# Kernel tuning notes

Hardware: AMD Instinct MI355X
Metric: run time of the kernel (lower is better)

Reference implementation:

```python
import jax, jax.numpy as jnp
import numpy as np
from jax import lax

BN_EPS = 1e-5

def conv_bn_prelu(x, w, b, scale, bias, a):
    # Conv2d(k=3, pad=1, stride=1) in NCHW / OIHW layout
    y = lax.conv_general_dilated(x, w, window_strides=(1, 1), padding='SAME',
                                 dimension_numbers=('NCHW', 'OIHW', 'NCHW'))
    y = y + b[None, :, None, None]
    # BatchNorm2d, training-mode batch statistics over (B, H, W)
    mean = jnp.mean(y, axis=(0, 2, 3), keepdims=True)
    var = jnp.var(y, axis=(0, 2, 3), keepdims=True)
    y = (y - mean) * lax.rsqrt(var + BN_EPS)
    y = y * scale[None, :, None, None] + bias[None, :, None, None]
    # PReLU with single shared slope parameter
    return jnp.where(y >= 0, y, a * y)

def setup_inputs() -> dict:
    key = jax.random.key(0)
    ks = jax.random.split(key, 7)
    B, C, H, W = 4, 64, 64, 64
    x = jax.random.normal(ks[0], (B, C, H, W), dtype=jnp.float32)
    conv_w = jax.random.normal(ks[1], (C, C, 3, 3), dtype=jnp.float32) * 0.05
    conv_b = jax.random.normal(ks[2], (C,), dtype=jnp.float32) * 0.05
    bn_scale = jax.random.uniform(ks[3], (C,), dtype=jnp.float32, minval=0.5, maxval=1.5)
    bn_bias = jax.random.normal(ks[4], (C,), dtype=jnp.float32) * 0.05
    prelu_a = jnp.full((1,), 0.25, dtype=jnp.float32)
    gamma = jax.random.normal(ks[5], (1,), dtype=jnp.float32)
    return {'x': x, 'conv_w': conv_w, 'conv_b': conv_b, 'bn_scale': bn_scale,
            'bn_bias': bn_bias, 'prelu_a': prelu_a, 'gamma': gamma}

def reference(x, conv_w, conv_b, bn_scale, bn_bias, prelu_a, gamma):
    B, C, H, W = x.shape
    N = H * W
    feat = conv_bn_prelu(x, conv_w, conv_b, bn_scale, bn_bias, prelu_a)  # (B,C,H,W)
    f = feat.reshape(B, C, N)  # proj_query = f^T, proj_key = f, proj_value = f
    # energy[b,i,j] = sum_c f[b,c,i] * f[b,c,j]  -> (B, N, N)
    energy = jnp.einsum('bci,bcj->bij', f, f)
    # energy_new = rowmax - energy, softmax over last dim
    energy_new = jnp.max(energy, axis=-1, keepdims=True) - energy
    attn = jax.nn.softmax(energy_new, axis=-1)
    # out = bmm(proj_value, attention^T): out[b,c,i] = sum_j f[b,c,j] * attn[b,i,j]
    out = jnp.einsum('bcj,bij->bci', f, attn).reshape(B, C, H, W)
    return gamma * out + feat
```

## Files before the change

### kernel.cpp

```cpp
#include <hip/hip_runtime.h>

constexpr int kB = 4, kC = 64, kH = 64, kW = 64, kN = kH * kW;
constexpr float kEps = 1e-5f;
constexpr float kQS = 1.2011224087864498f;

#if __has_builtin(__builtin_amdgcn_exp2f)
#define EXP2F(x) __builtin_amdgcn_exp2f(x)
#else
#define EXP2F(x) exp2f(x)
#endif

typedef __attribute__((ext_vector_type(8))) short short8;
typedef __attribute__((ext_vector_type(4))) float f32x4;
typedef unsigned short u16;

__device__ inline unsigned pkbf(float a, float b) {
  unsigned ua = __float_as_uint(a), ub = __float_as_uint(b);
  ua += 0x7fff + ((ua >> 16) & 1);
  ub += 0x7fff + ((ub >> 16) & 1);
  return (ua >> 16) | (ub & 0xffff0000u);
}

__global__ __launch_bounds__(256) void prep_w_kernel(const float* __restrict__ w,
                                                     u16* __restrict__ wA,
                                                     float* __restrict__ stat) {
  if (blockIdx.x == 0) {
    stat[threadIdx.x] = 0.f;
    stat[256 + threadIdx.x] = 0.f;
  }
  int idx = blockIdx.x * 256 + threadIdx.x;
  if (idx < 64 * 576) {
    int oc = idx / 576, r = idx - oc * 576;
    int khw = r >> 6, ic = r & 63;
    float v = w[(oc * 64 + ic) * 9 + khw];
    unsigned u = __float_as_uint(v);
    u += 0x7fff + ((u >> 16) & 1);
    wA[idx] = (u16)(u >> 16);
  }
}

__global__ __launch_bounds__(256) void conv_kernel(const float* __restrict__ x,
                                                   const u16* __restrict__ wA,
                                                   const float* __restrict__ bias,
                                                   float* __restrict__ y,
                                                   float* __restrict__ stat) {
  const int tid = threadIdx.x;
  const int lane = tid & 63;
  const int wv = tid >> 6;
  const int bx = blockIdx.x;
  const int b = bx >> 7;
  const int h = (bx & 127) >> 1;
  const int w0 = (bx & 1) * 32;
  const int lw = lane & 15, lg = lane >> 4;

  __shared__ __align__(16) u16 xt[3 * 40 * 64];

#pragma unroll
  for (int rep = 0; rep < 4; ++rep) {
    int idx = rep * 256 + tid;
    if (idx < 960) {
      int kh = idx / 320;
      int t = idx - kh * 320;
      int gw = t >> 5, icp = t & 31;
      int wb = w0 - 4 + gw * 4;
      int hh = h + kh - 1;
      float4 va = {0.f, 0.f, 0.f, 0.f}, vb = {0.f, 0.f, 0.f, 0.f};
      if (hh >= 0 && hh < 64 && wb >= 0 && wb < 64) {
        va = *(const float4*)&x[((b * 64 + icp * 2) * 64 + hh) * 64 + wb];
        vb = *(const float4*)&x[((b * 64 + icp * 2 + 1) * 64 + hh) * 64 + wb];
      }
      float av[4] = {va.x, va.y, va.z, va.w};
      float bv[4] = {vb.x, vb.y, vb.z, vb.w};
#pragma unroll
      for (int j = 0; j < 4; ++j) {
        int wc = gw * 4 + j;
        *(unsigned*)&xt[(kh * 40 + wc) * 64 + (((icp >> 2) ^ (wc & 7)) * 8 + (icp & 3) * 2)] =
            pkbf(av[j], bv[j]);
      }
    }
  }
  __syncthreads();

  const int oc0 = wv * 16;
  short8 af[18];
#pragma unroll
  for (int kc = 0; kc < 18; ++kc)
    af[kc] = *(const short8*)&wA[(oc0 + lw) * 576 + kc * 32 + lg * 8];

  f32x4 acc[2];
  acc[0] = (f32x4){0.f, 0.f, 0.f, 0.f};
  acc[1] = (f32x4){0.f, 0.f, 0.f, 0.f};
#pragma unroll
  for (int kc = 0; kc < 18; ++kc) {
    const int khw = kc >> 1;
    const int kh = khw / 3, kwv = khw % 3;
#pragma unroll
    for (int nt = 0; nt < 2; ++nt) {
      int wc = nt * 16 + lw + kwv + 3;
      short8 bf = *(const short8*)&xt[(kh * 40 + wc) * 64 + ((((kc & 1) * 4 + lg) ^ (wc & 7)) * 8)];
      acc[nt] = __builtin_amdgcn_mfma_f32_16x16x32_bf16(af[kc], bf, acc[nt], 0, 0, 0);
    }
  }

  float* st = stat + (bx & 3) * 128;
#pragma unroll
  for (int r = 0; r < 4; ++r) {
    const int oc = oc0 + lg * 4 + r;
    const float bz = bias[oc];
    float v0 = acc[0][r] + bz;
    float v1 = acc[1][r] + bz;
    y[((b * 64 + oc) * 64 + h) * 64 + w0 + lw] = v0;
    y[((b * 64 + oc) * 64 + h) * 64 + w0 + 16 + lw] = v1;
    float s = v0 + v1, q = v0 * v0 + v1 * v1;
#pragma unroll
    for (int m = 1; m < 16; m <<= 1) {
      s += __shfl_xor(s, m);
      q += __shfl_xor(q, m);
    }
    if (lw == 0) {
      atomicAdd(&st[oc], s);
      atomicAdd(&st[64 + oc], q);
    }
  }
}

__global__ __launch_bounds__(256) void pack_kernel(const float* __restrict__ y,
                                                   const float* __restrict__ stat,
                                                   const float* __restrict__ scale,
                                                   const float* __restrict__ bias,
                                                   const float* __restrict__ pa,
                                                   float* __restrict__ ABg,
                                                   u16* __restrict__ fbfA,
                                                   u16* __restrict__ fbfB) {
  __shared__ float ls[64 * 65];
  __shared__ float sAB[128];
  const int tid = threadIdx.x;
  const int b = blockIdx.x >> 6;
  const int n0 = (blockIdx.x & 63) << 6;
  if (tid < 64) {
    const float inv_n = 1.f / (float)(kB * kN);
    float ssum = stat[tid] + stat[128 + tid] + stat[256 + tid] + stat[384 + tid];
    float qsum = stat[64 + tid] + stat[192 + tid] + stat[320 + tid] + stat[448 + tid];
    float mean = ssum * inv_n;
    float var = qsum * inv_n - mean * mean;
    float A = scale[tid] * rsqrtf(var + kEps);
    float Bc = bias[tid] - mean * A;
    sAB[tid] = A;
    sAB[64 + tid] = Bc;
    ABg[tid] = A;
    ABg[64 + tid] = Bc;
  }
  __syncthreads();
  {
    const int c = tid >> 2, nj = (tid & 3) << 4;
    const float A = sAB[c], Bc = sAB[64 + c], a = pa[0];
    const float* yp = y + ((b * kC + c) * kN) + n0 + nj;
    float f[16];
#pragma unroll
    for (int v = 0; v < 4; ++v) {
      float4 xv = *(const float4*)(yp + v * 4);
      float t;
      t = fmaf(A, xv.x, Bc); f[v * 4 + 0] = t >= 0.f ? t : a * t;
      t = fmaf(A, xv.y, Bc); f[v * 4 + 1] = t >= 0.f ? t : a * t;
      t = fmaf(A, xv.z, Bc); f[v * 4 + 2] = t >= 0.f ? t : a * t;
      t = fmaf(A, xv.w, Bc); f[v * 4 + 3] = t >= 0.f ? t : a * t;
    }
#pragma unroll
    for (int v = 0; v < 16; ++v) ls[c * 65 + nj + v] = f[v];
  }
  __syncthreads();
  {
    int chunk = tid >> 5, pt = chunk >> 1, kc = chunk & 1;
    int lp2 = (tid & 31) * 2;
    u16* dst = fbfA + ((size_t)((b * 256 + (n0 >> 4) + pt) * 2 + kc)) * 512;
#pragma unroll
    for (int e = 0; e < 2; ++e) {
      int L = lp2 + e;
      int n = pt * 16 + (L & 15);
      int cb = kc * 32 + (L >> 4) * 8;
      float v[8];
#pragma unroll
      for (int r = 0; r < 8; ++r) v[r] = kQS * ls[(cb + r) * 65 + n];
      uint4 o = {pkbf(v[0], v[1]), pkbf(v[2], v[3]), pkbf(v[4], v[5]), pkbf(v[6], v[7])};
      *(uint4*)&dst[L * 8] = o;
    }
  }
  {
    int chunk = tid >> 5, jt = chunk >> 2, ct = chunk & 3;
    int lp2 = (tid & 31) * 2;
    u16* dst = fbfB + ((size_t)((b * 128 + (n0 >> 5) + jt) * 4 + ct)) * 512;
#pragma unroll
    for (int e = 0; e < 2; ++e) {
      int L = lp2 + e;
      int c = ct * 16 + (L & 15);
      int nb = jt * 32 + (L >> 4) * 8;
      float v[8];
#pragma unroll
      for (int r = 0; r < 8; ++r) v[r] = ls[c * 65 + nb + r];
      uint4 o = {pkbf(v[0], v[1]), pkbf(v[2], v[3]), pkbf(v[4], v[5]), pkbf(v[6], v[7])};
      *(uint4*)&dst[L * 8] = o;
    }
  }
}

__global__ __launch_bounds__(512, 1) void attn_kernel(const u16* __restrict__ fbfA,
                                                      const u16* __restrict__ fbfB,
                                                      const float* y,
                                                      const float* __restrict__ ABg,
                                                      const float* __restrict__ pa,
                                                      const float* __restrict__ gamma_p,
                                                      float* out) {
  const int tid = threadIdx.x;
  const int lane = tid & 63;
  const int w = tid >> 6;
  const int bx = blockIdx.x;
  const int b = bx >> 6, it4 = bx & 63;
  const int c15 = lane & 15, g = lane >> 4;

  __shared__ __align__(16) float Red[20480];
  u16* ps = (u16*)Red + w * 2560;
  const int pw_off = c15 * 40 + g * 4;
  const int pr_off = c15 * 40 + g * 8;

  const uint4* fA = (const uint4*)fbfA;
  const uint4* fB = (const uint4*)fbfB;

  uint4 qf[4][2];
#pragma unroll
  for (int it = 0; it < 4; ++it)
#pragma unroll
    for (int kc = 0; kc < 2; ++kc) {
      uint4 q = fA[(size_t)((b * 256 + it4 * 4 + it) * 2 + kc) * 64 + lane];
      q.x ^= 0x80008000u; q.y ^= 0x80008000u; q.z ^= 0x80008000u; q.w ^= 0x80008000u;
      qf[it][kc] = q;
    }

  const short8 ones = {0x3F80, 0x3F80, 0x3F80, 0x3F80, 0x3F80, 0x3F80, 0x3F80, 0x3F80};

  f32x4 oacc[4][4];
  f32x4 lacc[4];
#pragma unroll
  for (int it = 0; it < 4; ++it) {
    lacc[it] = (f32x4){0.f, 0.f, 0.f, 0.f};
#pragma unroll
    for (int ct = 0; ct < 4; ++ct) oacc[it][ct] = (f32x4){0.f, 0.f, 0.f, 0.f};
  }

#pragma unroll 2
  for (int jj2 = 0; jj2 < 16; ++jj2) {
    const int jj = jj2 * 8 + w;
    const int ca = (b * 256 + jj * 2) * 2;
    uint4 a00 = fA[(size_t)(ca + 0) * 64 + lane];
    uint4 a01 = fA[(size_t)(ca + 1) * 64 + lane];
    uint4 a10 = fA[(size_t)(ca + 2) * 64 + lane];
    uint4 a11 = fA[(size_t)(ca + 3) * 64 + lane];
    const int cb = (b * 128 + jj) * 4;
    uint4 v0 = fB[(size_t)(cb + 0) * 64 + lane];
    uint4 v1 = fB[(size_t)(cb + 1) * 64 + lane];
    uint4 v2 = fB[(size_t)(cb + 2) * 64 + lane];
    uint4 v3 = fB[(size_t)(cb + 3) * 64 + lane];

    f32x4 sv[2][4];
    __builtin_amdgcn_s_setprio(1);
#pragma unroll
    for (int it = 0; it < 4; ++it) {
      f32x4 z0 = (f32x4){0.f, 0.f, 0.f, 0.f};
      z0 = __builtin_amdgcn_mfma_f32_16x16x32_bf16(*(short8*)&a00, *(short8*)&qf[it][0], z0, 0, 0, 0);
      z0 = __builtin_amdgcn_mfma_f32_16x16x32_bf16(*(short8*)&a01, *(short8*)&qf[it][1], z0, 0, 0, 0);
      sv[0][it] = z0;
      f32x4 z1 = (f32x4){0.f, 0.f, 0.f, 0.f};
      z1 = __builtin_amdgcn_mfma_f32_16x16x32_bf16(*(short8*)&a10, *(short8*)&qf[it][0], z1, 0, 0, 0);
      z1 = __builtin_amdgcn_mfma_f32_16x16x32_bf16(*(short8*)&a11, *(short8*)&qf[it][1], z1, 0, 0, 0);
      sv[1][it] = z1;
    }
    __builtin_amdgcn_s_setprio(0);
#pragma unroll
    for (int it = 0; it < 4; ++it)
#pragma unroll
      for (int jt = 0; jt < 2; ++jt) {
        float p0 = EXP2F(sv[jt][it][0]);
        float p1 = EXP2F(sv[jt][it][1]);
        float p2 = EXP2F(sv[jt][it][2]);
        float p3 = EXP2F(sv[jt][it][3]);
        uint2 d;
        d.x = __builtin_amdgcn_perm(__float_as_uint(p1), __float_as_uint(p0), 0x07060302u);
        d.y = __builtin_amdgcn_perm(__float_as_uint(p3), __float_as_uint(p2), 0x07060302u);
        *(uint2*)&ps[pw_off + it * 640 + jt * 16] = d;
      }
    __builtin_amdgcn_s_setprio(1);
#pragma unroll
    for (int it = 0; it < 4; ++it) {
      short8 pf = *(const short8*)&ps[pr_off + it * 640];
      lacc[it] = __builtin_amdgcn_mfma_f32_16x16x32_bf16(pf, ones, lacc[it], 0, 0, 0);
      oacc[it][0] = __builtin_amdgcn_mfma_f32_16x16x32_bf16(pf, *(short8*)&v0, oacc[it][0], 0, 0, 0);
      oacc[it][1] = __builtin_amdgcn_mfma_f32_16x16x32_bf16(pf, *(short8*)&v1, oacc[it][1], 0, 0, 0);
      oacc[it][2] = __builtin_amdgcn_mfma_f32_16x16x32_bf16(pf, *(short8*)&v2, oacc[it][2], 0, 0, 0);
      oacc[it][3] = __builtin_amdgcn_mfma_f32_16x16x32_bf16(pf, *(short8*)&v3, oacc[it][3], 0, 0, 0);
    }
    __builtin_amdgcn_s_setprio(0);
  }

  for (int half = 4; half >= 1; half >>= 1) {
    __syncthreads();
    if (w >= half && w < 2 * half) {
      float* dst = Red + (w - half) * 5120;
#pragma unroll
      for (int it = 0; it < 4; ++it) {
#pragma unroll
        for (int ct = 0; ct < 4; ++ct)
          *(f32x4*)&dst[(it * 4 + ct) * 256 + lane * 4] = oacc[it][ct];
        *(f32x4*)&dst[(16 + it) * 256 + lane * 4] = lacc[it];
      }
    }
    __syncthreads();
    if (w < half) {
      const float* src = Red + w * 5120;
#pragma unroll
      for (int it = 0; it < 4; ++it) {
#pragma unroll
        for (int ct = 0; ct < 4; ++ct)
          oacc[it][ct] = oacc[it][ct] + *(const f32x4*)&src[(it * 4 + ct) * 256 + lane * 4];
        lacc[it] = lacc[it] + *(const f32x4*)&src[(16 + it) * 256 + lane * 4];
      }
    }
  }

  float* tr = Red + 5120;
  if (w == 0) {
    const float gm = gamma_p[0];
#pragma unroll
    for (int it = 0; it < 4; ++it) {
      f32x4 sc;
#pragma unroll
      for (int r = 0; r < 4; ++r) sc[r] = gm / lacc[it][r];
#pragma unroll
      for (int ct = 0; ct < 4; ++ct)
#pragma unroll
        for (int r = 0; r < 4; ++r)
          tr[(ct * 16 + c15) * 65 + it * 16 + g * 4 + r] = oacc[it][ct][r] * sc[r];
    }
  }
  __syncthreads();

  const float a = pa[0];
#pragma unroll
  for (int rr = 0; rr < 2; ++rr) {
    int flat4 = rr * 512 + tid;
    int c = flat4 >> 4, i4 = (flat4 & 15) * 4;
    const float A = ABg[c], Bc = ABg[64 + c];
    const size_t idx = (size_t)(b * 64 + c) * 4096 + it4 * 64 + i4;
    float4 yv = *(const float4*)&y[idx];
    float t;
    float4 ov;
    t = fmaf(A, yv.x, Bc); t = t >= 0.f ? t : a * t; ov.x = tr[c * 65 + i4 + 0] + t;
    t = fmaf(A, yv.y, Bc); t = t >= 0.f ? t : a * t; ov.y = tr[c * 65 + i4 + 1] + t;
    t = fmaf(A, yv.z, Bc); t = t >= 0.f ? t : a * t; ov.z = tr[c * 65 + i4 + 2] + t;
    t = fmaf(A, yv.w, Bc); t = t >= 0.f ? t : a * t; ov.w = tr[c * 65 + i4 + 3] + t;
    *(float4*)&out[idx] = ov;
  }
}

extern "C" void kernel_launch(void* const* d_in, const int* in_sizes, int n_in,
                              void* d_out, int out_size, void* d_ws, size_t ws_size,
                              hipStream_t stream) {
  (void)in_sizes; (void)n_in; (void)out_size; (void)ws_size;
  const float* x        = (const float*)d_in[0];
  const float* conv_w   = (const float*)d_in[1];
  const float* conv_b   = (const float*)d_in[2];
  const float* bn_scale = (const float*)d_in[3];
  const float* bn_bias  = (const float*)d_in[4];
  const float* prelu_a  = (const float*)d_in[5];
  const float* gamma    = (const float*)d_in[6];
  float* out = (float*)d_out;

  u16* fbfA = (u16*)d_ws;
  u16* fbfB = fbfA + kB * kC * kN;
  float* stat = (float*)(fbfB + kB * kC * kN);
  float* ABg = stat + 512;
  u16* wA = (u16*)(ABg + 128);

  float* y = out;

  prep_w_kernel<<<144, 256, 0, stream>>>(conv_w, wA, stat);
  conv_kernel<<<kB * kH * 2, 256, 0, stream>>>(x, wA, conv_b, y, stat);
  pack_kernel<<<kB * (kN / 64), 256, 0, stream>>>(y, stat, bn_scale, bn_bias, prelu_a,
                                                  ABg, fbfA, fbfB);
  attn_kernel<<<kB * 64, 512, 0, stream>>>(fbfA, fbfB, y, ABg, prelu_a, gamma, out);
}
```

Measured before the change: 115.8 us.

## Software-pipeline attention loop with double-buffered P tiles in LDS

Restructures the per-wave key loop into a two-stage software pipeline. The QK^T MFMAs and exp for the next key tile run while the PV MFMAs consume the previous tile's probabilities, which are read from a second LDS buffer. V fragments are prefetched one step ahead into alternating register sets. The aim is to overlap exp/VALU work and global loads with matrix ops. The cost is higher register pressure and twice the per-wave LDS scratch for P.

```diff
diff --git a/kernel.cpp b/kernel.cpp
--- a/kernel.cpp
+++ b/kernel.cpp
@@ -218,7 +218,8 @@
   const int c15 = lane & 15, g = lane >> 4;
 
   __shared__ __align__(16) float Red[20480];
-  u16* ps = (u16*)Red + w * 2560;
+  u16* psA = (u16*)Red + w * 2560;
+  u16* psB = (u16*)Red + 20480 + w * 2560;
   const int pw_off = c15 * 40 + g * 4;
   const int pr_off = c15 * 40 + g * 8;
 
@@ -246,20 +247,20 @@
     for (int ct = 0; ct < 4; ++ct) oacc[it][ct] = (f32x4){0.f, 0.f, 0.f, 0.f};
   }
 
-#pragma unroll 2
-  for (int jj2 = 0; jj2 < 16; ++jj2) {
-    const int jj = jj2 * 8 + w;
+  auto loadV = [&](int jj, uint4* vf) {
+    const int cb = (b * 128 + jj) * 4;
+    vf[0] = fB[(size_t)(cb + 0) * 64 + lane];
+    vf[1] = fB[(size_t)(cb + 1) * 64 + lane];
+    vf[2] = fB[(size_t)(cb + 2) * 64 + lane];
+    vf[3] = fB[(size_t)(cb + 3) * 64 + lane];
+  };
+
+  auto stage = [&](int jj, u16* psw) {
     const int ca = (b * 256 + jj * 2) * 2;
     uint4 a00 = fA[(size_t)(ca + 0) * 64 + lane];
     uint4 a01 = fA[(size_t)(ca + 1) * 64 + lane];
     uint4 a10 = fA[(size_t)(ca + 2) * 64 + lane];
     uint4 a11 = fA[(size_t)(ca + 3) * 64 + lane];
-    const int cb = (b * 128 + jj) * 4;
-    uint4 v0 = fB[(size_t)(cb + 0) * 64 + lane];
-    uint4 v1 = fB[(size_t)(cb + 1) * 64 + lane];
-    uint4 v2 = fB[(size_t)(cb + 2) * 64 + lane];
-    uint4 v3 = fB[(size_t)(cb + 3) * 64 + lane];
-
     f32x4 sv[2][4];
     __builtin_amdgcn_s_setprio(1);
 #pragma unroll
@@ -285,20 +286,50 @@
         uint2 d;
         d.x = __builtin_amdgcn_perm(__float_as_uint(p1), __float_as_uint(p0), 0x07060302u);
         d.y = __builtin_amdgcn_perm(__float_as_uint(p3), __float_as_uint(p2), 0x07060302u);
-        *(uint2*)&ps[pw_off + it * 640 + jt * 16] = d;
+        *(uint2*)&psw[pw_off + it * 640 + jt * 16] = d;
       }
+  };
+
+  auto pfread = [&](const u16* psw, short8* pf) {
+#pragma unroll
+    for (int it = 0; it < 4; ++it)
+      pf[it] = *(const short8*)&psw[pr_off + it * 640];
+  };
+
+  auto pvcompute = [&](const short8* pf, const uint4* vf) {
     __builtin_amdgcn_s_setprio(1);
 #pragma unroll
     for (int it = 0; it < 4; ++it) {
-      short8 pf = *(const short8*)&ps[pr_off + it * 640];
-      lacc[it] = __builtin_amdgcn_mfma_f32_16x16x32_bf16(pf, ones, lacc[it], 0, 0, 0);
-      oacc[it][0] = __builtin_amdgcn_mfma_f32_16x16x32_bf16(pf, *(short8*)&v0, oacc[it][0], 0, 0, 0);
-      oacc[it][1] = __builtin_amdgcn_mfma_f32_16x16x32_bf16(pf, *(short8*)&v1, oacc[it][1], 0, 0, 0);
-      oacc[it][2] = __builtin_amdgcn_mfma_f32_16x16x32_bf16(pf, *(short8*)&v2, oacc[it][2], 0, 0, 0);
-      oacc[it][3] = __builtin_amdgcn_mfma_f32_16x16x32_bf16(pf, *(short8*)&v3, oacc[it][3], 0, 0, 0);
+      lacc[it] = __builtin_amdgcn_mfma_f32_16x16x32_bf16(pf[it], ones, lacc[it], 0, 0, 0);
+      oacc[it][0] = __builtin_amdgcn_mfma_f32_16x16x32_bf16(pf[it], *(const short8*)&vf[0], oacc[it][0], 0, 0, 0);
+      oacc[it][1] = __builtin_amdgcn_mfma_f32_16x16x32_bf16(pf[it], *(const short8*)&vf[1], oacc[it][1], 0, 0, 0);
+      oacc[it][2] = __builtin_amdgcn_mfma_f32_16x16x32_bf16(pf[it], *(const short8*)&vf[2], oacc[it][2], 0, 0, 0);
+      oacc[it][3] = __builtin_amdgcn_mfma_f32_16x16x32_bf16(pf[it], *(const short8*)&vf[3], oacc[it][3], 0, 0, 0);
     }
     __builtin_amdgcn_s_setprio(0);
-  }
+  };
+
+  uint4 vf0[4], vf1[4];
+  short8 pf[4];
+
+  loadV(w, vf0);
+  stage(w, psA);
+  for (int p = 0; p < 7; ++p) {
+    pfread(psA, pf);
+    loadV((2 * p + 1) * 8 + w, vf1);
+    stage((2 * p + 1) * 8 + w, psB);
+    pvcompute(pf, vf0);
+    pfread(psB, pf);
+    loadV((2 * p + 2) * 8 + w, vf0);
+    stage((2 * p + 2) * 8 + w, psA);
+    pvcompute(pf, vf1);
+  }
+  pfread(psA, pf);
+  loadV(15 * 8 + w, vf1);
+  stage(15 * 8 + w, psB);
+  pvcompute(pf, vf0);
+  pfread(psB, pf);
+  pvcompute(pf, vf1);
 
   for (int half = 4; half >= 1; half >>= 1) {
     __syncthreads();
```

Measured after the change: 116.6 us. About the same (+0.7%).
